# Kernel optimization log

Measured on AMD Instinct MI355X. Metric: run time of the kernel, lower is better.

The kernel has to match this reference:

```python
import jax, jax.numpy as jnp
import numpy as np
from jax.scipy.linalg import solve_triangular

B, H, W, C, K = 8, 256, 256, 8, 16  # batch, height, width, channel_num, class_num


def setup_inputs() -> dict:
    key = jax.random.key(0)
    k1, k2, k3 = jax.random.split(key, 3)
    x = jax.random.normal(k1, (B, H, W, C), dtype=jnp.float32)
    # scale_tril weights: small random lower-ish matrix + identity on diag for
    # numerically sane Gaussian pdfs (layer init is 'uniform' near zero; we
    # shift the diagonal so probs are finite but the math is identical).
    scale = (0.1 * jax.random.normal(k2, (K, 1, C, C), dtype=jnp.float32)
             + jnp.eye(C, dtype=jnp.float32)[None, None])
    mean = 0.05 * jax.random.normal(k3, (K, 1, C), dtype=jnp.float32)
    return {"x": x, "scale": scale, "mean": mean}


def _forward(x, scale, mean):
    b = x.shape[0]
    hw = H * W
    xf = x.reshape(b, hw, C)                     # [B, HW, C]
    L = scale[:, 0]                               # [K, C, C] (lower tri used)
    mu = mean[:, 0]                               # [K, C]

    # MultivariateNormalTriL.prob: q = ||L^{-1}(x-mu)||^2, computed once per
    # (class, pixel) without tiling L/mu across pixels.
    diff = xf[None] - mu[:, None, None, :]        # [K, B, HW, C]
    d = diff.reshape(K, b * hw, C).transpose(0, 2, 1)  # [K, C, B*HW]
    y = solve_triangular(L, d, lower=True)        # [K, C, B*HW]
    quad = jnp.sum(y * y, axis=1)                 # [K, B*HW]
    log_det = jnp.sum(jnp.log(jnp.abs(jnp.diagonal(L, axis1=1, axis2=2))), axis=1)  # [K]
    log2pi = jnp.log(jnp.asarray(2.0 * np.pi, dtype=x.dtype))
    logp = -0.5 * quad - log_det[:, None] - 0.5 * C * log2pi
    gauss = jnp.exp(logp).reshape(K, b, hw)       # [K, B, HW]

    # output[i*C + j] = gauss[i] * x[..., j]  -> [K, C, B, HW]
    x_ch = xf.transpose(2, 0, 1)                  # [C, B, HW]
    outs = gauss[:, None, :, :] * x_ch[None]      # [K, C, B, HW]
    # Faithful to tf.reshape([K*C, B, HW] -> [B, H, W, K*C]) raw row-major reshape
    out = outs.reshape(K * C, b, hw).reshape(b, H, W, K * C)
    return jnp.concatenate([x.reshape(b, H, W, C), out], axis=3)


def reference(x, scale, mean):
    return _forward(x, scale, mean)
```

## Files before the change

kernel.cpp:

```cpp
#include <hip/hip_runtime.h>

#define S_TOTAL 524288u
#define NEG4LOG2PI (-7.3515082656373808f)

typedef float f32x4 __attribute__((ext_vector_type(4)));

__global__ void prep_kernel(const float* __restrict__ scale,
                            float* __restrict__ minv,
                            float* __restrict__ base) {
    int k = threadIdx.x;
    if (k >= 16) return;
    float L[8][8], M[8][8];
    const float* Ls = scale + k * 64;
    for (int i = 0; i < 8; i++)
        for (int j = 0; j < 8; j++) { L[i][j] = Ls[i * 8 + j]; M[i][j] = 0.f; }
    for (int j = 0; j < 8; j++) {
        M[j][j] = 1.0f / L[j][j];
        for (int i = j + 1; i < 8; i++) {
            float s = 0.f;
            for (int m = j; m < i; m++) s += L[i][m] * M[m][j];
            M[i][j] = -s / L[i][i];
        }
    }
    float logdet = 0.f;
    for (int i = 0; i < 8; i++) logdet += logf(fabsf(L[i][i]));
    for (int i = 0; i < 8; i++)
        for (int j = 0; j < 8; j++) minv[k * 64 + i * 8 + j] = M[i][j];
    base[k] = -logdet + NEG4LOG2PI;
}

__global__ __launch_bounds__(256) void gauss_xt_kernel(
    const float* __restrict__ x,
    const float* __restrict__ minv,
    const float* __restrict__ base,
    const float* __restrict__ mean,
    float* __restrict__ gauss,
    float* __restrict__ xt)
{
    __shared__ float sM[1024];
    __shared__ float sMu[128];
    __shared__ float sB[16];
    for (int i = threadIdx.x; i < 1024; i += 256) sM[i] = minv[i];
    if (threadIdx.x < 128) sMu[threadIdx.x] = mean[threadIdx.x];
    if (threadIdx.x < 16)  sB[threadIdx.x] = base[threadIdx.x];
    __syncthreads();

    unsigned s = blockIdx.x * 256u + threadIdx.x;
    f32x4 a = ((const f32x4*)x)[s * 2u];
    f32x4 b = ((const f32x4*)x)[s * 2u + 1u];
    float xv[8] = {a.x, a.y, a.z, a.w, b.x, b.y, b.z, b.w};

    #pragma unroll
    for (int c = 0; c < 8; c++) xt[c * S_TOTAL + s] = xv[c];

    #pragma unroll
    for (int k = 0; k < 16; k++) {
        const float* M  = &sM[k * 64];
        const float* mu = &sMu[k * 8];
        float d[8];
        #pragma unroll
        for (int c = 0; c < 8; c++) d[c] = xv[c] - mu[c];
        float quad = 0.f;
        #pragma unroll
        for (int i = 0; i < 8; i++) {
            float y = 0.f;
            #pragma unroll
            for (int j = 0; j <= i; j++) y = fmaf(M[i * 8 + j], d[j], y);
            quad = fmaf(y, y, quad);
        }
        gauss[k * S_TOTAL + s] = __expf(fmaf(-0.5f, quad, sB[k]));
    }
}

__global__ __launch_bounds__(256) void out_sweep_kernel(
    const float* __restrict__ x,
    const float* __restrict__ gauss,
    const float* __restrict__ xt,
    float* __restrict__ out)
{
    const unsigned t   = threadIdx.x;
    const unsigned b   = blockIdx.x;
    const unsigned kc  = b >> 5;
    const unsigned k   = kc >> 3, c = kc & 7u;
    const unsigned rb  = (b & 31u) * 128u;
    const unsigned q0  = kc * 4096u + rb;

    const f32x4* __restrict__ gk = (const f32x4*)(gauss + (size_t)k * S_TOTAL) + rb * 32u;
    const f32x4* __restrict__ xc = (const f32x4*)(xt    + (size_t)c * S_TOTAL) + rb * 32u;
    const f32x4* __restrict__ xh = (const f32x4*)(x + (size_t)q0 * 8u);
    f32x4* __restrict__ o = (f32x4*)(out + (size_t)q0 * 136u);

    #pragma unroll
    for (unsigned pass = 0; pass < 17u; ++pass) {
        unsigned i   = pass * 256u + t;
        unsigned r   = i / 34u;
        unsigned ch4 = i - r * 34u;
        f32x4 v;
        if (ch4 < 2u) {
            v = xh[r * 2u + ch4];
        } else {
            unsigned idx = r * 32u + (ch4 - 2u);
            v = gk[idx] * xc[idx];
        }
        __builtin_nontemporal_store(v, o + i);
    }
}

__global__ __launch_bounds__(256) void fused_kernel(
    const float* __restrict__ x,
    const float* __restrict__ mean,
    const float* __restrict__ scale,
    float* __restrict__ out)
{
    __shared__ float sM[1024];
    __shared__ float sMu[128];
    __shared__ float sB[16];
    __shared__ float sXrT[8][128];
    __shared__ float sGT[16][128];
    __shared__ float sXq[128][8];

    const unsigned t  = threadIdx.x;
    const unsigned r0 = blockIdx.x;

    if (t < 16u) {
        float L[8][8], M[8][8];
        const float* Ls = scale + t * 64u;
        for (int i = 0; i < 8; i++)
            for (int j = 0; j < 8; j++) { L[i][j] = Ls[i * 8 + j]; M[i][j] = 0.f; }
        for (int j = 0; j < 8; j++) {
            M[j][j] = 1.0f / L[j][j];
            for (int i = j + 1; i < 8; i++) {
                float s = 0.f;
                for (int m = j; m < i; m++) s += L[i][m] * M[m][j];
                M[i][j] = -s / L[i][i];
            }
        }
        float logdet = 0.f;
        for (int i = 0; i < 8; i++) logdet += logf(fabsf(L[i][i]));
        for (int i = 0; i < 8; i++)
            for (int j = 0; j < 8; j++) sM[t * 64u + i * 8 + j] = M[i][j];
        sB[t] = -logdet + NEG4LOG2PI;
    }
    if (t < 128u) sMu[t] = mean[t];

    {
        f32x4 v = ((const f32x4*)x)[r0 * 256u + t];
        unsigned p = t >> 1, h = (t & 1u) * 4u;
        sXrT[h + 0][p] = v.x; sXrT[h + 1][p] = v.y;
        sXrT[h + 2][p] = v.z; sXrT[h + 3][p] = v.w;
    }
    {
        unsigned kc = t >> 1, h = t & 1u;
        f32x4 v = ((const f32x4*)x)[(kc * 4096u + r0) * 2u + h];
        unsigned bofs = h * 4u;
        sXq[kc][bofs + 0] = v.x; sXq[kc][bofs + 1] = v.y;
        sXq[kc][bofs + 2] = v.z; sXq[kc][bofs + 3] = v.w;
    }
    __syncthreads();

    {
        unsigned j  = t & 127u;
        unsigned k0 = (t >> 7) * 8u;
        float xv[8];
        #pragma unroll
        for (int c = 0; c < 8; c++) xv[c] = sXrT[c][j];
        #pragma unroll
        for (unsigned kk = 0; kk < 8u; kk++) {
            unsigned k = k0 + kk;
            const float* M  = &sM[k * 64u];
            const float* mu = &sMu[k * 8u];
            float d[8];
            #pragma unroll
            for (int c = 0; c < 8; c++) d[c] = xv[c] - mu[c];
            float quad = 0.f;
            #pragma unroll
            for (int i = 0; i < 8; i++) {
                float y = 0.f;
                #pragma unroll
                for (int jj = 0; jj <= i; jj++) y = fmaf(M[i * 8 + jj], d[jj], y);
                quad = fmaf(y, y, quad);
            }
            sGT[k][j] = __expf(fmaf(-0.5f, quad, sB[k]));
        }
    }
    __syncthreads();

    for (unsigned i = t; i < 4352u; i += 256u) {
        unsigned kc = i / 34u;
        unsigned f4 = i - kc * 34u;
        f32x4 v;
        if (f4 < 2u) {
            v = *(const f32x4*)&sXq[kc][f4 * 4u];
        } else {
            unsigned j0 = f4 * 4u - 8u;
            unsigned k  = kc >> 3, c = kc & 7u;
            f32x4 g  = *(const f32x4*)&sGT[k][j0];
            f32x4 xcv = *(const f32x4*)&sXrT[c][j0];
            v = g * xcv;
        }
        float* dst = out + (kc * 4096u + r0) * 136u + f4 * 4u;
        __builtin_nontemporal_store(v, (f32x4*)dst);
    }
}

extern "C" void kernel_launch(void* const* d_in, const int* in_sizes, int n_in,
                              void* d_out, int out_size, void* d_ws, size_t ws_size,
                              hipStream_t stream) {
    const float* x     = (const float*)d_in[0];
    const float* scale = (const float*)d_in[1];
    const float* mean  = (const float*)d_in[2];
    float* out = (float*)d_out;

    const size_t GAUSS_BYTES = (size_t)16 * S_TOTAL * 4;
    const size_t XT_BYTES    = (size_t)8  * S_TOTAL * 4;
    const size_t NEED = GAUSS_BYTES + XT_BYTES + (1024 + 16) * sizeof(float);

    if (ws_size >= NEED) {
        float* gauss = (float*)d_ws;
        float* xt    = (float*)((char*)d_ws + GAUSS_BYTES);
        float* minv  = (float*)((char*)d_ws + GAUSS_BYTES + XT_BYTES);
        float* base  = minv + 1024;
        prep_kernel<<<1, 64, 0, stream>>>(scale, minv, base);
        gauss_xt_kernel<<<S_TOTAL / 256, 256, 0, stream>>>(x, minv, base, mean, gauss, xt);
        out_sweep_kernel<<<4096, 256, 0, stream>>>(x, gauss, xt, out);
    } else {
        fused_kernel<<<4096, 256, 0, stream>>>(x, mean, scale, out);
    }
}
```

Measured before the change: 314.6 us.

## Process four pixels per thread in gauss kernel and use regular output stores

The gauss/xt kernel now handles four consecutive pixels per thread, so xt and gauss writes become 16-byte vector stores instead of scalar strided stores, with a quarter as many blocks. The out sweep and fused kernels replace nontemporal stores with ordinary stores, and in the fused kernel with four scalar stores. The intent is to cut store transaction count in the intermediate kernel, at the cost of more registers per thread and fewer threads in flight. Dropping nontemporal hints may let the large output stream pollute caches.

```diff
diff --git a/kernel.cpp b/kernel.cpp
--- a/kernel.cpp
+++ b/kernel.cpp
@@ -45,30 +45,43 @@
     if (threadIdx.x < 16)  sB[threadIdx.x] = base[threadIdx.x];
     __syncthreads();
 
-    unsigned s = blockIdx.x * 256u + threadIdx.x;
-    f32x4 a = ((const f32x4*)x)[s * 2u];
-    f32x4 b = ((const f32x4*)x)[s * 2u + 1u];
-    float xv[8] = {a.x, a.y, a.z, a.w, b.x, b.y, b.z, b.w};
-
-    #pragma unroll
-    for (int c = 0; c < 8; c++) xt[c * S_TOTAL + s] = xv[c];
+    const unsigned p0 = (blockIdx.x * 256u + threadIdx.x) * 4u;
+    float xv[4][8];
+    #pragma unroll
+    for (int p = 0; p < 4; p++) {
+        f32x4 a = ((const f32x4*)x)[(p0 + p) * 2u];
+        f32x4 b = ((const f32x4*)x)[(p0 + p) * 2u + 1u];
+        xv[p][0] = a.x; xv[p][1] = a.y; xv[p][2] = a.z; xv[p][3] = a.w;
+        xv[p][4] = b.x; xv[p][5] = b.y; xv[p][6] = b.z; xv[p][7] = b.w;
+    }
+
+    #pragma unroll
+    for (int c = 0; c < 8; c++) {
+        f32x4 v = {xv[0][c], xv[1][c], xv[2][c], xv[3][c]};
+        *(f32x4*)&xt[c * S_TOTAL + p0] = v;
+    }
 
     #pragma unroll
     for (int k = 0; k < 16; k++) {
         const float* M  = &sM[k * 64];
         const float* mu = &sMu[k * 8];
-        float d[8];
+        f32x4 g;
         #pragma unroll
-        for (int c = 0; c < 8; c++) d[c] = xv[c] - mu[c];
-        float quad = 0.f;
-        #pragma unroll
-        for (int i = 0; i < 8; i++) {
-            float y = 0.f;
-            #pragma unroll
-            for (int j = 0; j <= i; j++) y = fmaf(M[i * 8 + j], d[j], y);
-            quad = fmaf(y, y, quad);
-        }
-        gauss[k * S_TOTAL + s] = __expf(fmaf(-0.5f, quad, sB[k]));
+        for (int p = 0; p < 4; p++) {
+            float d[8];
+            #pragma unroll
+            for (int c = 0; c < 8; c++) d[c] = xv[p][c] - mu[c];
+            float quad = 0.f;
+            #pragma unroll
+            for (int i = 0; i < 8; i++) {
+                float y = 0.f;
+                #pragma unroll
+                for (int j = 0; j <= i; j++) y = fmaf(M[i * 8 + j], d[j], y);
+                quad = fmaf(y, y, quad);
+            }
+            g[p] = __expf(fmaf(-0.5f, quad, sB[k]));
+        }
+        *(f32x4*)&gauss[k * S_TOTAL + p0] = g;
     }
 }
 
@@ -102,7 +115,7 @@
             unsigned idx = r * 32u + (ch4 - 2u);
             v = gk[idx] * xc[idx];
         }
-        __builtin_nontemporal_store(v, o + i);
+        o[i] = v;
     }
 }
 
@@ -198,8 +211,10 @@
             f32x4 xcv = *(const f32x4*)&sXrT[c][j0];
             v = g * xcv;
         }
-        float* dst = out + (kc * 4096u + r0) * 136u + f4 * 4u;
-        __builtin_nontemporal_store(v, (f32x4*)dst);
+        out[(kc * 4096u + r0) * 136u + f4 * 4u + 0] = v.x;
+        out[(kc * 4096u + r0) * 136u + f4 * 4u + 1] = v.y;
+        out[(kc * 4096u + r0) * 136u + f4 * 4u + 2] = v.z;
+        out[(kc * 4096u + r0) * 136u + f4 * 4u + 3] = v.w;
     }
 }
 
@@ -221,7 +236,7 @@
         float* minv  = (float*)((char*)d_ws + GAUSS_BYTES + XT_BYTES);
         float* base  = minv + 1024;
         prep_kernel<<<1, 64, 0, stream>>>(scale, minv, base);
-        gauss_xt_kernel<<<S_TOTAL / 256, 256, 0, stream>>>(x, minv, base, mean, gauss, xt);
+        gauss_xt_kernel<<<S_TOTAL / 4 / 256, 256, 0, stream>>>(x, minv, base, mean, gauss, xt);
         out_sweep_kernel<<<4096, 256, 0, stream>>>(x, gauss, xt, out);
     } else {
         fused_kernel<<<4096, 256, 0, stream>>>(x, mean, scale, out);
```

Result: slower. 347.5 us (+10.4%).
